# Kernel optimization log

Hardware: AMD Instinct MI355X
Metric: run time of the kernel (lower is better)

Reference implementation:

```python
import jax, jax.numpy as jnp
import numpy as np

B, T, E, H = 2, 2048, 1024, 4
Dk = E // H          # 256 head qk dim
Dv = Dk * 2          # 512 head v dim (expansion_ratio=2)
EPS = 1e-5
ROPE_BASE = 10000.0


def setup_inputs() -> dict:
    key = jax.random.key(0)
    ks = jax.random.split(key, 7)
    s = 0.02  # small init matching xavier gains in reset_parameters
    return {
        "x": jax.random.normal(ks[0], (B, T, E), jnp.float32),
        "Wq": jax.random.normal(ks[1], (E, E), jnp.float32) * s,
        "Wk": jax.random.normal(ks[2], (E, E), jnp.float32) * s,
        "Wv": jax.random.normal(ks[3], (E, 2 * E), jnp.float32) * s,
        "Wg": jax.random.normal(ks[4], (E, 2 * E), jnp.float32) * s,
        "Wo": jax.random.normal(ks[5], (2 * E, E), jnp.float32) * s,
        "gn_weight": jnp.ones((Dv,), jnp.float32),
    }


def _rotary(q, k):
    # q,k: [b, t, h, d]; non-interleaved (GPT-NeoX) rotary over the full head dim
    d = q.shape[-1]
    inv_freq = 1.0 / (ROPE_BASE ** (jnp.arange(0, d, 2, dtype=jnp.float32) / d))
    t = jnp.arange(q.shape[1], dtype=jnp.float32)
    freqs = jnp.einsum('t,f->tf', t, inv_freq)      # [t, d/2]
    cos = jnp.cos(freqs)[None, :, None, :]
    sin = jnp.sin(freqs)[None, :, None, :]

    def rot(x):
        x1, x2 = x[..., : d // 2], x[..., d // 2:]
        return jnp.concatenate([x1 * cos - x2 * sin, x2 * cos + x1 * sin], axis=-1)

    return rot(q), rot(k)


def reference(x, Wq, Wk, Wv, Wg, Wo, gn_weight):
    b, t, e = x.shape
    q = (x @ Wq).reshape(b, t, H, Dk)
    k = (x @ Wk).reshape(b, t, H, Dk)
    q, k = _rotary(q, k)
    q = q.transpose(0, 2, 1, 3) * (Dk ** -0.5)      # [b,h,t,dk], scale = head_qk_dim^-0.5
    k = k.transpose(0, 2, 1, 3)
    v = (x @ Wv).reshape(b, t, H, Dv).transpose(0, 2, 1, 3)  # [b,h,t,dv]

    # RetNet per-head decay: gamma_h = 1 - 2^-(5+h)
    gamma = 1.0 - jnp.exp2(-5.0 - jnp.arange(H, dtype=jnp.float32))
    ti = jnp.arange(t)
    n = ti[:, None] - ti[None, :]                   # t - s
    decay = jnp.where(
        n >= 0,
        gamma[:, None, None] ** jnp.maximum(n, 0).astype(jnp.float32),
        0.0,
    )                                               # [h,t,t] causal decayed mask

    scores = jnp.einsum('bhtd,bhsd->bhts', q, k) * decay[None]
    o = jnp.einsum('bhts,bhsd->bhtd', scores, v)    # [b,h,t,dv]
    o = o.transpose(0, 2, 1, 3)                     # [b,t,h,dv]

    # per-head RMSNorm (group_norm over head_v_dim)
    rms = jnp.sqrt(jnp.mean(o * o, axis=-1, keepdims=True) + EPS)
    o = o / rms * gn_weight

    # NOTE: the given source multiplies by raw g_proj(x) (gate_fn not applied in forward)
    g = x @ Wg                                      # [b,t,2E]
    return (o.reshape(b, t, H * Dv) * g) @ Wo       # [b,t,E]
```

## Files before the change

### kernel.cpp

```cpp
#include <hip/hip_runtime.h>
#include <hip/hip_bf16.h>

#define B_ 2
#define T_ 2048
#define E_ 1024
#define DK 256
#define DV 512
#define MROWS 4096
#define LDQKVG 6144
#define CHK 128
#define NCHK 16

typedef __attribute__((ext_vector_type(8))) short short8;
typedef __attribute__((ext_vector_type(4))) short short4v;
typedef __attribute__((ext_vector_type(4))) float floatx4;

typedef __attribute__((address_space(3))) unsigned as3_u32;
typedef const __attribute__((address_space(1))) unsigned as1_u32;

static __device__ __forceinline__ void gld_lds16(const unsigned short* gsrc, unsigned short* ldst) {
  __builtin_amdgcn_global_load_lds((as1_u32*)gsrc, (as3_u32*)ldst, 16, 0, 0);
}

static __device__ __forceinline__ float bf2f(unsigned short u) {
  union { unsigned int i; float f; } x; x.i = ((unsigned int)u) << 16; return x.f;
}
static __device__ __forceinline__ unsigned short f2bf(float f) {
  __hip_bfloat16 h = __float2bfloat16(f);
  return __builtin_bit_cast(unsigned short, h);
}
static __device__ __forceinline__ float load_as_f(const float* p) { return *p; }
static __device__ __forceinline__ float load_as_f(const unsigned short* p) { return bf2f(*p); }

__global__ void __launch_bounds__(256) convx_kernel(const float* __restrict__ x,
                                                    unsigned short* __restrict__ xb) {
  int i = blockIdx.x * 256 + threadIdx.x;
  size_t base = (size_t)i * 8;
  float4 a = *(const float4*)(x + base);
  float4 b = *(const float4*)(x + base + 4);
  short8 o;
  o[0] = (short)f2bf(a.x); o[1] = (short)f2bf(a.y);
  o[2] = (short)f2bf(a.z); o[3] = (short)f2bf(a.w);
  o[4] = (short)f2bf(b.x); o[5] = (short)f2bf(b.y);
  o[6] = (short)f2bf(b.z); o[7] = (short)f2bf(b.w);
  *(short8*)(xb + base) = o;
}

template<typename TIN>
__global__ void __launch_bounds__(256) transpose_bf16_kernel(
    const TIN* __restrict__ in, int ldin, unsigned short* __restrict__ out, int ldout) {
  __shared__ float tile[32][33];
  int c0 = blockIdx.x * 32, r0 = blockIdx.y * 32;
  int tx = threadIdx.x & 31, ty = threadIdx.x >> 5;
#pragma unroll
  for (int i = 0; i < 32; i += 8)
    tile[ty + i][tx] = load_as_f(&in[(size_t)(r0 + ty + i) * ldin + c0 + tx]);
  __syncthreads();
#pragma unroll
  for (int i = 0; i < 32; i += 8)
    out[(size_t)(c0 + ty + i) * ldout + r0 + tx] = f2bf(tile[tx][ty + i]);
}

__global__ void __launch_bounds__(256) transpose_weights_kernel(
    const float* __restrict__ Wq, const float* __restrict__ Wk,
    const float* __restrict__ Wv, const float* __restrict__ Wg,
    unsigned short* __restrict__ out) {
  __shared__ float tile[32][33];
  int bid = blockIdx.x;
  const float* in; unsigned short* o; int ldin, nbx;
  if (bid < 1024)      { in = Wq; o = out;                       ldin = 1024; nbx = 32; }
  else if (bid < 2048) { in = Wk; o = out + (size_t)1024 * 1024; ldin = 1024; nbx = 32; bid -= 1024; }
  else if (bid < 4096) { in = Wv; o = out + (size_t)2048 * 1024; ldin = 2048; nbx = 64; bid -= 2048; }
  else                 { in = Wg; o = out + (size_t)4096 * 1024; ldin = 2048; nbx = 64; bid -= 4096; }
  int c0 = (bid % nbx) * 32, r0 = (bid / nbx) * 32;
  int tx = threadIdx.x & 31, ty = threadIdx.x >> 5;
#pragma unroll
  for (int i = 0; i < 32; i += 8)
    tile[ty + i][tx] = in[(size_t)(r0 + ty + i) * ldin + c0 + tx];
  __syncthreads();
#pragma unroll
  for (int i = 0; i < 32; i += 8)
    o[(size_t)(c0 + ty + i) * 1024 + r0 + tx] = f2bf(tile[tx][ty + i]);
}

__global__ void __launch_bounds__(256) kts_transpose_kernel(
    const unsigned short* __restrict__ in, unsigned short* __restrict__ out) {
  __shared__ float tile[32][33];
  int c0 = blockIdx.x * 32, r0 = blockIdx.y * 32;
  int tx = threadIdx.x & 31, ty = threadIdx.x >> 5;
#pragma unroll
  for (int i = 0; i < 32; i += 8)
    tile[ty + i][tx] = bf2f(in[(size_t)(r0 + ty + i) * LDQKVG + c0 + tx]);
  __syncthreads();
  int h = c0 >> 8;
  float lg = log2f(1.0f - exp2f(-5.0f - (float)h));
  int t = r0 + tx;
  float fac = exp2f((float)(CHK - (t & (CHK - 1))) * lg);
#pragma unroll
  for (int i = 0; i < 32; i += 8)
    out[(size_t)(c0 + ty + i) * MROWS + r0 + tx] = f2bf(tile[tx][ty + i] * fac);
}

template<int BM, int BN, int WM_W, int WN_W, int MINW, bool F32OUT>
__global__ void __launch_bounds__(WM_W * WN_W * 64, MINW) gemmp_kernel(
    const unsigned short* __restrict__ A, int lda,
    const unsigned short* __restrict__ Bt, int ldb, int K,
    void* __restrict__ Cp, int ldc, int ccol0, int nbx) {
  constexpr int WAVES = WM_W * WN_W;
  constexpr int AG = BM / 16 / WAVES;
  constexpr int BG = BN / 16 / WAVES;
  constexpr int RM = BM / WM_W;
  constexpr int CN = BN / WN_W;
  constexpr int MB = RM / 16, NB = CN / 16;
  __shared__ __align__(16) unsigned short lds[3][(BM + BN) * 32];
  const int tid = threadIdx.x;
  const int lane = tid & 63;
  const int wid = tid >> 6;
  const int wm = wid / WN_W, wn = wid % WN_W;
  const int q8 = gridDim.x >> 3;
  const int bid = (blockIdx.x & 7) * q8 + (blockIdx.x >> 3);
  const int m0 = (bid % nbx) * BM;
  const int n0 = (bid / nbx) * BN;
  const unsigned short* Ab = A + (size_t)m0 * lda;
  const unsigned short* Bb = Bt + (size_t)n0 * ldb;
  const int NT = K / 32;

  auto stage = [&](int sl, int t) {
    const int k0 = t * 32;
#pragma unroll
    for (int j = 0; j < AG; ++j) {
      int g = wid * AG + j;
      int ci = g * 64 + lane;
      int row = ci >> 2, c = ci & 3;
      int cs = c ^ ((row >> 1) & 3);
      gld_lds16(Ab + (size_t)row * lda + k0 + cs * 8, &lds[sl][g * 512]);
    }
#pragma unroll
    for (int j = 0; j < BG; ++j) {
      int g = wid * BG + j;
      int ci = g * 64 + lane;
      int row = ci >> 2, c = ci & 3;
      int cs = c ^ ((row >> 1) & 3);
      gld_lds16(Bb + (size_t)row * ldb + k0 + cs * 8, &lds[sl][BM * 32 + g * 512]);
    }
  };

  floatx4 acc[MB][NB];
#pragma unroll
  for (int i = 0; i < MB; i++)
#pragma unroll
    for (int j = 0; j < NB; j++)
      acc[i][j] = (floatx4){0.f, 0.f, 0.f, 0.f};

  stage(0, 0);
  stage(1, 1);

  int cur = 0;
#pragma unroll 1
  for (int t = 0; t < NT; ++t) {
    if (t + 1 < NT) {
      if constexpr (AG + BG == 2) asm volatile("s_waitcnt vmcnt(2)" ::: "memory");
      else if constexpr (AG + BG == 3) asm volatile("s_waitcnt vmcnt(3)" ::: "memory");
      else if constexpr (AG + BG == 4) asm volatile("s_waitcnt vmcnt(4)" ::: "memory");
      else if constexpr (AG + BG == 6) asm volatile("s_waitcnt vmcnt(6)" ::: "memory");
      else asm volatile("s_waitcnt vmcnt(8)" ::: "memory");
    } else {
      asm volatile("s_waitcnt vmcnt(0)" ::: "memory");
    }
    __builtin_amdgcn_s_barrier();
    asm volatile("" ::: "memory");
    int sl = cur + 2; if (sl >= 3) sl -= 3;
    if (t + 2 < NT) stage(sl, t + 2);

    const unsigned short* As_ = lds[cur];
    const unsigned short* Bs_ = lds[cur] + BM * 32;
    short8 af[MB], bfv[NB];
#pragma unroll
    for (int i = 0; i < MB; ++i) {
      int row = wm * RM + i * 16 + (lane & 15);
      af[i] = *(const short8*)&As_[row * 32 + (((lane >> 4) ^ ((row >> 1) & 3)) * 8)];
    }
#pragma unroll
    for (int j = 0; j < NB; ++j) {
      int nn = wn * CN + j * 16 + (lane & 15);
      bfv[j] = *(const short8*)&Bs_[nn * 32 + (((lane >> 4) ^ ((nn >> 1) & 3)) * 8)];
    }
#pragma unroll
    for (int i = 0; i < MB; ++i)
#pragma unroll
      for (int j = 0; j < NB; ++j)
        acc[i][j] = __builtin_amdgcn_mfma_f32_16x16x32_bf16(af[i], bfv[j], acc[i][j], 0, 0, 0);
    cur = cur + 1 == 3 ? 0 : cur + 1;
  }

#pragma unroll
  for (int i = 0; i < MB; ++i)
#pragma unroll
    for (int j = 0; j < NB; ++j)
#pragma unroll
      for (int r = 0; r < 4; ++r) {
        int row = m0 + wm * RM + i * 16 + (lane >> 4) * 4 + r;
        int col = ccol0 + n0 + wn * CN + j * 16 + (lane & 15);
        float v = acc[i][j][r];
        if (F32OUT) ((float*)Cp)[(size_t)row * ldc + col] = v;
        else ((unsigned short*)Cp)[(size_t)row * ldc + col] = f2bf(v);
      }
}

__global__ void __launch_bounds__(256) rope_table_kernel(float2* __restrict__ tab) {
  int idx = blockIdx.x * 256 + threadIdx.x;
  int t = idx >> 7, j = idx & 127;
  float invf = exp2f(-(float)j * (13.287712379549449f / 128.0f));
  float ang = (float)t * invf;
  tab[idx] = make_float2(cosf(ang), sinf(ang));
}

__global__ void __launch_bounds__(256) rope_kernel(unsigned short* __restrict__ qkvg,
                                                   const float2* __restrict__ tab) {
  int idx = blockIdx.x * 256 + threadIdx.x;
  int jv = idx & 15;
  int h = (idx >> 4) & 3;
  int row = idx >> 6;
  int t = row & (T_ - 1);
  int j0 = jv * 8;
  float lg = log2f(1.0f - exp2f(-5.0f - (float)h));
  float sq = 0.0625f * exp2f((float)(t & (CHK - 1)) * lg);
  size_t base = (size_t)row * LDQKVG + h * DK + j0;
  short8 q1 = *(const short8*)&qkvg[base],      q2 = *(const short8*)&qkvg[base + 128];
  short8 k1 = *(const short8*)&qkvg[base + E_], k2 = *(const short8*)&qkvg[base + E_ + 128];
  short8 oq1, oq2, ok1, ok2;
#pragma unroll
  for (int e = 0; e < 8; ++e) {
    float2 cs = tab[(t << 7) + j0 + e];
    float c = cs.x, s = cs.y;
    float a1 = bf2f((unsigned short)q1[e]), a2 = bf2f((unsigned short)q2[e]);
    float b1 = bf2f((unsigned short)k1[e]), b2 = bf2f((unsigned short)k2[e]);
    oq1[e] = (short)f2bf((a1 * c - a2 * s) * sq);
    oq2[e] = (short)f2bf((a2 * c + a1 * s) * sq);
    ok1[e] = (short)f2bf(b1 * c - b2 * s);
    ok2[e] = (short)f2bf(b2 * c + b1 * s);
  }
  *(short8*)&qkvg[base]            = oq1;
  *(short8*)&qkvg[base + 128]      = oq2;
  *(short8*)&qkvg[base + E_]       = ok1;
  *(short8*)&qkvg[base + E_ + 128] = ok2;
}

__global__ void __launch_bounds__(256) state_kernel(
    const unsigned short* __restrict__ kTs, const unsigned short* __restrict__ vT,
    unsigned short* __restrict__ Sbuf) {
  const int lane = threadIdx.x & 63, wid = threadIdx.x >> 6;
  const int bh = blockIdx.x & 7, dkt = (blockIdx.x >> 3) & 3, dvt = (blockIdx.x >> 5) & 15;
  const int b = bh >> 2, h = bh & 3;
  const float lg = log2f(1.0f - exp2f(-5.0f - (float)h));
  const float g128 = exp2f((float)CHK * lg);
  const int dk0 = dkt * 64 + wid * 16;
  const int dv0 = dvt * 32;
  const unsigned short* arow = kTs + (size_t)(h * DK + dk0 + (lane & 15)) * MROWS + b * T_ + (lane >> 4) * 8;
  const unsigned short* brow = vT + (size_t)(h * DV + dv0 + (lane & 15)) * MROWS + b * T_ + (lane >> 4) * 8;
  floatx4 acc[2];
  acc[0] = (floatx4){0.f, 0.f, 0.f, 0.f};
  acc[1] = (floatx4){0.f, 0.f, 0.f, 0.f};
#pragma unroll 4
  for (int c = 0; c < NCHK; ++c) {
    size_t sb = (size_t)(c * 8 + bh) * (DV * DK);
#pragma unroll
    for (int nb = 0; nb < 2; ++nb) {
      short4v o;
#pragma unroll
      for (int r = 0; r < 4; ++r) o[r] = (short)f2bf(acc[nb][r]);
      *(short4v*)&Sbuf[sb + (size_t)(dv0 + nb * 16 + (lane & 15)) * DK + dk0 + (lane >> 4) * 4] = o;
    }
#pragma unroll
    for (int nb = 0; nb < 2; ++nb)
#pragma unroll
      for (int r = 0; r < 4; ++r) acc[nb][r] *= g128;
#pragma unroll
    for (int ks = 0; ks < 4; ++ks) {
      short8 a = *(const short8*)(arow + c * CHK + ks * 32);
#pragma unroll
      for (int nb = 0; nb < 2; ++nb) {
        short8 bb = *(const short8*)(brow + (size_t)nb * 16 * MROWS + c * CHK + ks * 32);
        acc[nb] = __builtin_amdgcn_mfma_f32_16x16x32_bf16(a, bb, acc[nb], 0, 0, 0);
      }
    }
  }
}

__global__ void __launch_bounds__(256) retention2_kernel(
    const unsigned short* __restrict__ qkvg, const unsigned short* __restrict__ vT,
    const unsigned short* __restrict__ Sbuf, const float* __restrict__ gnw,
    unsigned short* __restrict__ og, float* __restrict__ ssbuf) {
  __shared__ unsigned short k_lds[2][32 * 256];
  __shared__ unsigned short v_lds[2][256 * 32];
  __shared__ unsigned short s_lds[4][16 * 40];
  const int tid = threadIdx.x, lane = tid & 63, wid = tid >> 6;
  const int bh  = blockIdx.x & 7;
  const int c   = (blockIdx.x >> 3) & 15;
  const int dvh = (blockIdx.x >> 7) & 1;
  const int rhf = (blockIdx.x >> 8) & 1;
  const int b = bh >> 2, h = bh & 3;
  const float lg = log2f(1.0f - exp2f(-5.0f - (float)h));
  const int rb0 = b * T_ + c * CHK + rhf * 64;
  const int taub = rhf * 64 + wid * 16;
  const int nst = rhf ? 4 : 2;
  const unsigned short* kbase = qkvg + (size_t)(b * T_ + c * CHK) * LDQKVG + E_ + h * DK;
  const unsigned short* vbase = vT + (size_t)(h * DV + dvh * 256) * MROWS + b * T_ + c * CHK;
  const unsigned short* Sp = Sbuf + (size_t)(c * 8 + bh) * (DV * DK) + (size_t)dvh * 256 * DK;

  auto stage = [&](int buf, int st) {
    int s0 = st * 32;
#pragma unroll
    for (int j = 0; j < 4; ++j) {
      int ci = (wid * 4 + j) * 64 + lane;
      int row = ci >> 5, cc = ci & 31;
      int cs = cc ^ (row & 7);
      gld_lds16(kbase + (size_t)(s0 + row) * LDQKVG + cs * 8, &k_lds[buf][(wid * 4 + j) * 512]);
    }
#pragma unroll
    for (int j = 0; j < 4; ++j) {
      int ci = (wid * 4 + j) * 64 + lane;
      int dv = ci >> 2, cc = ci & 3;
      int cs = cc ^ ((dv ^ (dv >> 2)) & 3);
      gld_lds16(vbase + (size_t)dv * MROWS + s0 + cs * 8, &v_lds[buf][(wid * 4 + j) * 512]);
    }
  };

  stage(0, 0);

  short8 qf[8];
  {
    int qrow = rb0 + wid * 16 + (lane & 15);
    const unsigned short* qp = qkvg + (size_t)qrow * LDQKVG + h * DK + (lane >> 4) * 8;
#pragma unroll
    for (int kk = 0; kk < 8; kk++) qf[kk] = *(const short8*)(qp + kk * 32);
  }
  floatx4 oacc[16];
#pragma unroll
  for (int nb = 0; nb < 16; ++nb) oacc[nb] = (floatx4){0.f, 0.f, 0.f, 0.f};
#pragma unroll
  for (int ks = 0; ks < 8; ++ks) {
#pragma unroll
    for (int nb = 0; nb < 16; ++nb) {
      short8 sf = *(const short8*)&Sp[(size_t)(nb * 16 + (lane & 15)) * DK + ks * 32 + (lane >> 4) * 8];
      oacc[nb] = __builtin_amdgcn_mfma_f32_16x16x32_bf16(qf[ks], sf, oacc[nb], 0, 0, 0);
    }
  }

#pragma unroll 1
  for (int st = 0; st < nst; ++st) {
    const int cur = st & 1;
    __syncthreads();
    if (st + 1 < nst) stage(cur ^ 1, st + 1);
#pragma unroll
    for (int ch = 0; ch < 2; ++ch) {
      floatx4 f = (floatx4){0.f, 0.f, 0.f, 0.f};
      const int srow = ch * 16 + (lane & 15);
#pragma unroll
      for (int kk = 0; kk < 8; kk++) {
        int cc = (kk * 4 + (lane >> 4)) ^ (srow & 7);
        short8 kf = *(const short8*)&k_lds[cur][srow * 256 + cc * 8];
        f = __builtin_amdgcn_mfma_f32_16x16x32_bf16(qf[kk], kf, f, 0, 0, 0);
      }
#pragma unroll
      for (int r = 0; r < 4; ++r) {
        int lr = (lane >> 4) * 4 + r;
        int sig = st * 32 + ch * 16 + (lane & 15);
        int n = taub + lr - sig;
        float val = (n >= 0) ? f[r] * exp2f(-(float)sig * lg) : 0.0f;
        s_lds[wid][lr * 40 + ch * 16 + (lane & 15)] = f2bf(val);
      }
    }
    short8 af = *(const short8*)&s_lds[wid][(lane & 15) * 40 + (lane >> 4) * 8];
#pragma unroll
    for (int nb = 0; nb < 16; ++nb) {
      int dv = nb * 16 + (lane & 15);
      int cc = (lane >> 4) ^ ((dv ^ (dv >> 2)) & 3);
      short8 vf = *(const short8*)&v_lds[cur][dv * 32 + cc * 8];
      oacc[nb] = __builtin_amdgcn_mfma_f32_16x16x32_bf16(af, vf, oacc[nb], 0, 0, 0);
    }
  }
#pragma unroll
  for (int r = 0; r < 4; ++r) {
    float ss = 0.f;
#pragma unroll
    for (int nb = 0; nb < 16; nb++) { float xv = oacc[nb][r]; ss += xv * xv; }
    ss += __shfl_xor(ss, 1, 64);
    ss += __shfl_xor(ss, 2, 64);
    ss += __shfl_xor(ss, 4, 64);
    ss += __shfl_xor(ss, 8, 64);
    if ((lane & 15) == 0) {
      int row = rb0 + wid * 16 + (lane >> 4) * 4 + r;
      ssbuf[(size_t)row * 8 + h * 2 + dvh] = ss;
    }
  }
#pragma unroll
  for (int r = 0; r < 4; ++r) {
    int row = rb0 + wid * 16 + (lane >> 4) * 4 + r;
    size_t growbase = (size_t)row * LDQKVG + 4096 + h * DV + dvh * 256;
    size_t orowbase = (size_t)row * LDQKVG + h * DV + dvh * 256;
#pragma unroll
    for (int nb = 0; nb < 16; nb++) {
      int col = nb * 16 + (lane & 15);
      float gv = bf2f(qkvg[growbase + col]);
      og[orowbase + col] = f2bf(oacc[nb][r] * gnw[dvh * 256 + col] * gv);
    }
  }
}

__global__ void __launch_bounds__(256) normalize_kernel(
    unsigned short* __restrict__ og, const float* __restrict__ ssbuf) {
  int i = blockIdx.x * 256 + threadIdx.x;
  size_t e0 = (size_t)i * 8;
  int row = (int)(e0 >> 11);
  int col = (int)(e0 & 2047);
  int h = col >> 9;
  float ss = ssbuf[(size_t)row * 8 + h * 2] + ssbuf[(size_t)row * 8 + h * 2 + 1];
  float inv = rsqrtf(ss * (1.0f / 512.0f) + 1e-5f);
  size_t a = (size_t)row * LDQKVG + col;
  short8 v = *(const short8*)(og + a);
#pragma unroll
  for (int j = 0; j < 8; j++) v[j] = (short)f2bf(bf2f((unsigned short)v[j]) * inv);
  *(short8*)(og + a) = v;
}

extern "C" void kernel_launch(void* const* d_in, const int* in_sizes, int n_in,
                              void* d_out, int out_size, void* d_ws, size_t ws_size,
                              hipStream_t stream) {
  const float* x   = (const float*)d_in[0];
  const float* Wq  = (const float*)d_in[1];
  const float* Wk  = (const float*)d_in[2];
  const float* Wv  = (const float*)d_in[3];
  const float* Wg  = (const float*)d_in[4];
  const float* Wo  = (const float*)d_in[5];
  const float* gnw = (const float*)d_in[6];
  float* out = (float*)d_out;

  char* ws = (char*)d_ws;
  size_t off = 0;
  auto alloc = [&](size_t bytes) { char* p = ws + off; off += (bytes + 255) & ~(size_t)255; return p; };
  unsigned short* qkvg = (unsigned short*)alloc((size_t)MROWS * LDQKVG * 2);
  unsigned short* vT   = (unsigned short*)alloc((size_t)2048 * MROWS * 2);
  char* regS = alloc((size_t)NCHK * 8 * DV * DK * 2);
  unsigned short* Sbuf  = (unsigned short*)regS;
  unsigned short* xb    = (unsigned short*)regS;
  unsigned short* WallT = (unsigned short*)(regS + 8388608);
  char* regK = alloc((size_t)1024 * MROWS * 2);
  unsigned short* kTs = (unsigned short*)regK;
  unsigned short* WoT = (unsigned short*)regK;
  float2* ropetab = (float2*)regK;
  float* ssbuf = (float*)alloc((size_t)MROWS * 8 * 4);
  unsigned short* og = qkvg + 2048;

  convx_kernel<<<2048, 256, 0, stream>>>(x, xb);

  transpose_weights_kernel<<<6144, 256, 0, stream>>>(Wq, Wk, Wv, Wg, WallT);

  rope_table_kernel<<<1024, 256, 0, stream>>>(ropetab);

  gemmp_kernel<128, 256, 2, 4, 4, false><<<768, 512, 0, stream>>>(
      xb, 1024, WallT, 1024, 1024, qkvg, LDQKVG, 0, 32);

  rope_kernel<<<1024, 256, 0, stream>>>(qkvg, ropetab);

  kts_transpose_kernel<<<dim3(32, 128), 256, 0, stream>>>(qkvg + E_, kTs);

  transpose_bf16_kernel<unsigned short><<<dim3(64, 128), 256, 0, stream>>>(qkvg + 2048, LDQKVG, vT, MROWS);

  state_kernel<<<512, 256, 0, stream>>>(kTs, vT, Sbuf);

  transpose_bf16_kernel<float><<<dim3(32, 64), 256, 0, stream>>>(Wo, 1024, WoT, 2048);

  retention2_kernel<<<512, 256, 0, stream>>>(qkvg, vT, Sbuf, gnw, og, ssbuf);

  normalize_kernel<<<4096, 256, 0, stream>>>(og, ssbuf);

  gemmp_kernel<128, 128, 2, 2, 3, true><<<256, 256, 0, stream>>>(
      og, LDQKVG, WoT, 2048, 2048, out, E_, 0, 32);
}
```

Measured before the change: 227.6 us.

## Fuse prep kernels and merge rope with K/V transposes into one pass

Merges the x conversion, weight transposes, rope table and Wo transpose into one prep launch. It also fuses the rope application with the decay-scaled K transpose and the V transpose into a single postproc kernel, so qkvg is read once instead of three times. Workspace regions that were aliased now get separate allocations. The GEMM block-index swizzle is removed, which may change L2 locality, and postproc uses large LDS buffers with only 512 blocks, which may limit occupancy.

Result: faster. 215.0 us (-5.6%).

```diff
diff --git a/kernel.cpp b/kernel.cpp
--- a/kernel.cpp
+++ b/kernel.cpp
@@ -29,76 +29,68 @@
   __hip_bfloat16 h = __float2bfloat16(f);
   return __builtin_bit_cast(unsigned short, h);
 }
-static __device__ __forceinline__ float load_as_f(const float* p) { return *p; }
-static __device__ __forceinline__ float load_as_f(const unsigned short* p) { return bf2f(*p); }
-
-__global__ void __launch_bounds__(256) convx_kernel(const float* __restrict__ x,
-                                                    unsigned short* __restrict__ xb) {
-  int i = blockIdx.x * 256 + threadIdx.x;
-  size_t base = (size_t)i * 8;
-  float4 a = *(const float4*)(x + base);
-  float4 b = *(const float4*)(x + base + 4);
-  short8 o;
-  o[0] = (short)f2bf(a.x); o[1] = (short)f2bf(a.y);
-  o[2] = (short)f2bf(a.z); o[3] = (short)f2bf(a.w);
-  o[4] = (short)f2bf(b.x); o[5] = (short)f2bf(b.y);
-  o[6] = (short)f2bf(b.z); o[7] = (short)f2bf(b.w);
-  *(short8*)(xb + base) = o;
-}
-
-template<typename TIN>
-__global__ void __launch_bounds__(256) transpose_bf16_kernel(
-    const TIN* __restrict__ in, int ldin, unsigned short* __restrict__ out, int ldout) {
-  __shared__ float tile[32][33];
-  int c0 = blockIdx.x * 32, r0 = blockIdx.y * 32;
-  int tx = threadIdx.x & 31, ty = threadIdx.x >> 5;
-#pragma unroll
-  for (int i = 0; i < 32; i += 8)
-    tile[ty + i][tx] = load_as_f(&in[(size_t)(r0 + ty + i) * ldin + c0 + tx]);
-  __syncthreads();
-#pragma unroll
-  for (int i = 0; i < 32; i += 8)
-    out[(size_t)(c0 + ty + i) * ldout + r0 + tx] = f2bf(tile[tx][ty + i]);
-}
-
-__global__ void __launch_bounds__(256) transpose_weights_kernel(
+
+__global__ void __launch_bounds__(256) prep_kernel(
+    const float* __restrict__ x, unsigned short* __restrict__ xb,
     const float* __restrict__ Wq, const float* __restrict__ Wk,
     const float* __restrict__ Wv, const float* __restrict__ Wg,
-    unsigned short* __restrict__ out) {
+    unsigned short* __restrict__ WallT,
+    const float* __restrict__ Wo, unsigned short* __restrict__ WoT,
+    float2* __restrict__ ropetab) {
   __shared__ float tile[32][33];
   int bid = blockIdx.x;
-  const float* in; unsigned short* o; int ldin, nbx;
-  if (bid < 1024)      { in = Wq; o = out;                       ldin = 1024; nbx = 32; }
-  else if (bid < 2048) { in = Wk; o = out + (size_t)1024 * 1024; ldin = 1024; nbx = 32; bid -= 1024; }
-  else if (bid < 4096) { in = Wv; o = out + (size_t)2048 * 1024; ldin = 2048; nbx = 64; bid -= 2048; }
-  else                 { in = Wg; o = out + (size_t)4096 * 1024; ldin = 2048; nbx = 64; bid -= 4096; }
-  int c0 = (bid % nbx) * 32, r0 = (bid / nbx) * 32;
-  int tx = threadIdx.x & 31, ty = threadIdx.x >> 5;
-#pragma unroll
-  for (int i = 0; i < 32; i += 8)
-    tile[ty + i][tx] = in[(size_t)(r0 + ty + i) * ldin + c0 + tx];
-  __syncthreads();
-#pragma unroll
-  for (int i = 0; i < 32; i += 8)
-    o[(size_t)(c0 + ty + i) * 1024 + r0 + tx] = f2bf(tile[tx][ty + i]);
-}
-
-__global__ void __launch_bounds__(256) kts_transpose_kernel(
-    const unsigned short* __restrict__ in, unsigned short* __restrict__ out) {
-  __shared__ float tile[32][33];
-  int c0 = blockIdx.x * 32, r0 = blockIdx.y * 32;
-  int tx = threadIdx.x & 31, ty = threadIdx.x >> 5;
-#pragma unroll
-  for (int i = 0; i < 32; i += 8)
-    tile[ty + i][tx] = bf2f(in[(size_t)(r0 + ty + i) * LDQKVG + c0 + tx]);
-  __syncthreads();
-  int h = c0 >> 8;
-  float lg = log2f(1.0f - exp2f(-5.0f - (float)h));
-  int t = r0 + tx;
-  float fac = exp2f((float)(CHK - (t & (CHK - 1))) * lg);
-#pragma unroll
-  for (int i = 0; i < 32; i += 8)
-    out[(size_t)(c0 + ty + i) * MROWS + r0 + tx] = f2bf(tile[tx][ty + i] * fac);
+  int tid = threadIdx.x;
+  if (bid < 2048) {
+    int i = bid * 256 + tid;
+    size_t base = (size_t)i * 8;
+    float4 a = *(const float4*)(x + base);
+    float4 b = *(const float4*)(x + base + 4);
+    short8 o;
+    o[0] = (short)f2bf(a.x); o[1] = (short)f2bf(a.y);
+    o[2] = (short)f2bf(a.z); o[3] = (short)f2bf(a.w);
+    o[4] = (short)f2bf(b.x); o[5] = (short)f2bf(b.y);
+    o[6] = (short)f2bf(b.z); o[7] = (short)f2bf(b.w);
+    *(short8*)(xb + base) = o;
+    return;
+  }
+  if (bid < 8192) {
+    bid -= 2048;
+    const float* in; unsigned short* o; int ldin, nbx;
+    if (bid < 1024)      { in = Wq; o = WallT;                       ldin = 1024; nbx = 32; }
+    else if (bid < 2048) { in = Wk; o = WallT + (size_t)1024 * 1024; ldin = 1024; nbx = 32; bid -= 1024; }
+    else if (bid < 4096) { in = Wv; o = WallT + (size_t)2048 * 1024; ldin = 2048; nbx = 64; bid -= 2048; }
+    else                 { in = Wg; o = WallT + (size_t)4096 * 1024; ldin = 2048; nbx = 64; bid -= 4096; }
+    int c0 = (bid % nbx) * 32, r0 = (bid / nbx) * 32;
+    int tx = tid & 31, ty = tid >> 5;
+#pragma unroll
+    for (int i = 0; i < 32; i += 8)
+      tile[ty + i][tx] = in[(size_t)(r0 + ty + i) * ldin + c0 + tx];
+    __syncthreads();
+#pragma unroll
+    for (int i = 0; i < 32; i += 8)
+      o[(size_t)(c0 + ty + i) * 1024 + r0 + tx] = f2bf(tile[tx][ty + i]);
+    return;
+  }
+  if (bid < 9216) {
+    int idx = (bid - 8192) * 256 + tid;
+    int t = idx >> 7, j = idx & 127;
+    float invf = exp2f(-(float)j * (13.287712379549449f / 128.0f));
+    float ang = (float)t * invf;
+    ropetab[idx] = make_float2(cosf(ang), sinf(ang));
+    return;
+  }
+  {
+    int lb = bid - 9216;
+    int c0 = (lb & 31) * 32, r0 = (lb >> 5) * 32;
+    int tx = tid & 31, ty = tid >> 5;
+#pragma unroll
+    for (int i = 0; i < 32; i += 8)
+      tile[ty + i][tx] = Wo[(size_t)(r0 + ty + i) * 1024 + c0 + tx];
+    __syncthreads();
+#pragma unroll
+    for (int i = 0; i < 32; i += 8)
+      WoT[(size_t)(c0 + ty + i) * 2048 + r0 + tx] = f2bf(tile[tx][ty + i]);
+  }
 }
 
 template<int BM, int BN, int WM_W, int WN_W, int MINW, bool F32OUT>
@@ -117,8 +109,7 @@
   const int lane = tid & 63;
   const int wid = tid >> 6;
   const int wm = wid / WN_W, wn = wid % WN_W;
-  const int q8 = gridDim.x >> 3;
-  const int bid = (blockIdx.x & 7) * q8 + (blockIdx.x >> 3);
+  const int bid = blockIdx.x;
   const int m0 = (bid % nbx) * BM;
   const int n0 = (bid / nbx) * BN;
   const unsigned short* Ab = A + (size_t)m0 * lda;
@@ -207,43 +198,81 @@
       }
 }
 
-__global__ void __launch_bounds__(256) rope_table_kernel(float2* __restrict__ tab) {
-  int idx = blockIdx.x * 256 + threadIdx.x;
-  int t = idx >> 7, j = idx & 127;
-  float invf = exp2f(-(float)j * (13.287712379549449f / 128.0f));
-  float ang = (float)t * invf;
-  tab[idx] = make_float2(cosf(ang), sinf(ang));
-}
-
-__global__ void __launch_bounds__(256) rope_kernel(unsigned short* __restrict__ qkvg,
-                                                   const float2* __restrict__ tab) {
-  int idx = blockIdx.x * 256 + threadIdx.x;
-  int jv = idx & 15;
-  int h = (idx >> 4) & 3;
-  int row = idx >> 6;
-  int t = row & (T_ - 1);
-  int j0 = jv * 8;
-  float lg = log2f(1.0f - exp2f(-5.0f - (float)h));
-  float sq = 0.0625f * exp2f((float)(t & (CHK - 1)) * lg);
-  size_t base = (size_t)row * LDQKVG + h * DK + j0;
-  short8 q1 = *(const short8*)&qkvg[base],      q2 = *(const short8*)&qkvg[base + 128];
-  short8 k1 = *(const short8*)&qkvg[base + E_], k2 = *(const short8*)&qkvg[base + E_ + 128];
-  short8 oq1, oq2, ok1, ok2;
-#pragma unroll
-  for (int e = 0; e < 8; ++e) {
-    float2 cs = tab[(t << 7) + j0 + e];
-    float c = cs.x, s = cs.y;
-    float a1 = bf2f((unsigned short)q1[e]), a2 = bf2f((unsigned short)q2[e]);
-    float b1 = bf2f((unsigned short)k1[e]), b2 = bf2f((unsigned short)k2[e]);
-    oq1[e] = (short)f2bf((a1 * c - a2 * s) * sq);
-    oq2[e] = (short)f2bf((a2 * c + a1 * s) * sq);
-    ok1[e] = (short)f2bf(b1 * c - b2 * s);
-    ok2[e] = (short)f2bf(b2 * c + b1 * s);
-  }
-  *(short8*)&qkvg[base]            = oq1;
-  *(short8*)&qkvg[base + 128]      = oq2;
-  *(short8*)&qkvg[base + E_]       = ok1;
-  *(short8*)&qkvg[base + E_ + 128] = ok2;
+__global__ void __launch_bounds__(256) postproc_kernel(
+    unsigned short* __restrict__ qkvg, const float2* __restrict__ tab,
+    unsigned short* __restrict__ kTs, unsigned short* __restrict__ vT) {
+  __shared__ unsigned short kt[256][33];
+  __shared__ unsigned short vt[512][33];
+  const int tid = threadIdx.x;
+  const int rt = blockIdx.x >> 2, h = blockIdx.x & 3;
+  const int grow0 = rt * 32;
+  const float lg = log2f(1.0f - exp2f(-5.0f - (float)h));
+  const int r = tid >> 3;
+  const int grow = grow0 + r;
+  const int t = grow & (T_ - 1);
+  const float sq = 0.0625f * exp2f((float)(t & (CHK - 1)) * lg);
+  const float fac = exp2f((float)(CHK - (t & (CHK - 1))) * lg);
+#pragma unroll
+  for (int half = 0; half < 2; ++half) {
+    int j0 = (tid & 7) * 8 + half * 64;
+    size_t base = (size_t)grow * LDQKVG + h * DK + j0;
+    short8 q1 = *(const short8*)&qkvg[base],      q2 = *(const short8*)&qkvg[base + 128];
+    short8 k1 = *(const short8*)&qkvg[base + E_], k2 = *(const short8*)&qkvg[base + E_ + 128];
+    short8 oq1, oq2, ok1, ok2;
+#pragma unroll
+    for (int e = 0; e < 8; ++e) {
+      float2 cs = tab[(t << 7) + j0 + e];
+      float c = cs.x, s = cs.y;
+      float a1 = bf2f((unsigned short)q1[e]), a2 = bf2f((unsigned short)q2[e]);
+      float b1 = bf2f((unsigned short)k1[e]), b2 = bf2f((unsigned short)k2[e]);
+      float rk1 = b1 * c - b2 * s, rk2 = b2 * c + b1 * s;
+      oq1[e] = (short)f2bf((a1 * c - a2 * s) * sq);
+      oq2[e] = (short)f2bf((a2 * c + a1 * s) * sq);
+      ok1[e] = (short)f2bf(rk1);
+      ok2[e] = (short)f2bf(rk2);
+      kt[j0 + e][r]       = f2bf(rk1 * fac);
+      kt[j0 + e + 128][r] = f2bf(rk2 * fac);
+    }
+    *(short8*)&qkvg[base]            = oq1;
+    *(short8*)&qkvg[base + 128]      = oq2;
+    *(short8*)&qkvg[base + E_]       = ok1;
+    *(short8*)&qkvg[base + E_ + 128] = ok2;
+  }
+  __syncthreads();
+  {
+    int dk = tid;
+    unsigned short* dst = kTs + (size_t)(h * DK + dk) * MROWS + grow0;
+#pragma unroll
+    for (int i = 0; i < 4; ++i) {
+      short8 w;
+#pragma unroll
+      for (int e = 0; e < 8; ++e) w[e] = (short)kt[dk][i * 8 + e];
+      *(short8*)(dst + i * 8) = w;
+    }
+  }
+  {
+    int cv = tid & 7;
+#pragma unroll
+    for (int i = 0; i < 8; ++i) {
+      int col = cv * 64 + i * 8;
+      short8 v = *(const short8*)&qkvg[(size_t)grow * LDQKVG + 2048 + h * DV + col];
+#pragma unroll
+      for (int e = 0; e < 8; ++e) vt[col + e][r] = (unsigned short)v[e];
+    }
+  }
+  __syncthreads();
+#pragma unroll
+  for (int p = 0; p < 2; ++p) {
+    int dv = p * 256 + tid;
+    unsigned short* dst = vT + (size_t)(h * DV + dv) * MROWS + grow0;
+#pragma unroll
+    for (int i = 0; i < 4; ++i) {
+      short8 w;
+#pragma unroll
+      for (int e = 0; e < 8; ++e) w[e] = (short)vt[dv][i * 8 + e];
+      *(short8*)(dst + i * 8) = w;
+    }
+  }
 }
 
 __global__ void __launch_bounds__(256) state_kernel(
@@ -445,31 +474,20 @@
   unsigned short* Sbuf  = (unsigned short*)regS;
   unsigned short* xb    = (unsigned short*)regS;
   unsigned short* WallT = (unsigned short*)(regS + 8388608);
-  char* regK = alloc((size_t)1024 * MROWS * 2);
-  unsigned short* kTs = (unsigned short*)regK;
-  unsigned short* WoT = (unsigned short*)regK;
-  float2* ropetab = (float2*)regK;
+  unsigned short* kTs = (unsigned short*)alloc((size_t)1024 * MROWS * 2);
+  unsigned short* WoT = (unsigned short*)alloc((size_t)1024 * 2048 * 2);
+  float2* ropetab = (float2*)alloc((size_t)T_ * 128 * 8);
   float* ssbuf = (float*)alloc((size_t)MROWS * 8 * 4);
   unsigned short* og = qkvg + 2048;
 
-  convx_kernel<<<2048, 256, 0, stream>>>(x, xb);
-
-  transpose_weights_kernel<<<6144, 256, 0, stream>>>(Wq, Wk, Wv, Wg, WallT);
-
-  rope_table_kernel<<<1024, 256, 0, stream>>>(ropetab);
+  prep_kernel<<<11264, 256, 0, stream>>>(x, xb, Wq, Wk, Wv, Wg, WallT, Wo, WoT, ropetab);
 
   gemmp_kernel<128, 256, 2, 4, 4, false><<<768, 512, 0, stream>>>(
       xb, 1024, WallT, 1024, 1024, qkvg, LDQKVG, 0, 32);
 
-  rope_kernel<<<1024, 256, 0, stream>>>(qkvg, ropetab);
-
-  kts_transpose_kernel<<<dim3(32, 128), 256, 0, stream>>>(qkvg + E_, kTs);
-
-  transpose_bf16_kernel<unsigned short><<<dim3(64, 128), 256, 0, stream>>>(qkvg + 2048, LDQKVG, vT, MROWS);
+  postproc_kernel<<<512, 256, 0, stream>>>(qkvg, ropetab, kTs, vT);
 
   state_kernel<<<512, 256, 0, stream>>>(kTs, vT, Sbuf);
-
-  transpose_bf16_kernel<float><<<dim3(32, 64), 256, 0, stream>>>(Wo, 1024, WoT, 2048);
 
   retention2_kernel<<<512, 256, 0, stream>>>(qkvg, vT, Sbuf, gnw, og, ssbuf);
 
```
